# Optimization experiments

Measured on AMD Instinct MI355X. Metric: run time of the kernel, lower is better.

Reference implementation:

```python
import jax, jax.numpy as jnp
import numpy as np

N, E, T = 6144, 98304, 32
D_IN, D, D_FF, H, OUT = 128, 256, 256, 4, 2
DH = D // H
EPS = 1e-5


def setup_inputs() -> dict:
    key = jax.random.key(0)
    ks = jax.random.split(key, 24)
    s = 0.05
    inp = {
        "x": jax.random.normal(ks[0], (N, D_IN), jnp.float32),
        "edge_index": jax.random.randint(ks[1], (2, E), 0, N, jnp.int64 if jax.config.jax_enable_x64 else jnp.int32),
        "timesteps": jnp.sort(jax.random.randint(ks[2], (N,), 0, T)),
        "lin_l_w": jax.random.normal(ks[3], (D, D_IN), jnp.float32) * s,
        "lin_l_b": jnp.zeros((D,), jnp.float32),
        "lin_r_w": jax.random.normal(ks[4], (D, D_IN), jnp.float32) * s,
        "bn_gamma": jnp.ones((D,), jnp.float32),
        "bn_beta": jnp.zeros((D,), jnp.float32),
        "in_proj_w": jax.random.normal(ks[5], (2, 3 * D, D), jnp.float32) * s,
        "in_proj_b": jnp.zeros((2, 3 * D), jnp.float32),
        "out_w": jax.random.normal(ks[6], (2, D, D), jnp.float32) * s,
        "out_b": jnp.zeros((2, D), jnp.float32),
        "ff1_w": jax.random.normal(ks[7], (2, D_FF, D), jnp.float32) * s,
        "ff1_b": jnp.zeros((2, D_FF), jnp.float32),
        "ff2_w": jax.random.normal(ks[8], (2, D, D_FF), jnp.float32) * s,
        "ff2_b": jnp.zeros((2, D), jnp.float32),
        "ln1_g": jnp.ones((2, D), jnp.float32),
        "ln1_b": jnp.zeros((2, D), jnp.float32),
        "ln2_g": jnp.ones((2, D), jnp.float32),
        "ln2_b": jnp.zeros((2, D), jnp.float32),
        "cls_w": jax.random.normal(ks[9], (OUT, D), jnp.float32) * s,
        "cls_b": jnp.zeros((OUT,), jnp.float32),
    }
    return inp


def _layernorm(h, g, b):
    mu = jnp.mean(h, -1, keepdims=True)
    v = jnp.var(h, -1, keepdims=True)
    return (h - mu) * jax.lax.rsqrt(v + EPS) * g + b


def _forward(x, edge_index, timesteps, lin_l_w, lin_l_b, lin_r_w, bn_gamma, bn_beta,
             in_proj_w, in_proj_b, out_w, out_b, ff1_w, ff1_b, ff2_w, ff2_b,
             ln1_g, ln1_b, ln2_g, ln2_b, cls_w, cls_b):
    # SAGEConv (mean aggregation): out = lin_l(mean_{j->i} x_j) + lin_r(x_i)
    src, dst = edge_index[0], edge_index[1]
    agg = jax.ops.segment_sum(x[src], dst, num_segments=N)
    cnt = jax.ops.segment_sum(jnp.ones((E,), x.dtype), dst, num_segments=N)
    agg = agg / jnp.maximum(cnt, 1.0)[:, None]
    h = agg @ lin_l_w.T + lin_l_b + x @ lin_r_w.T

    # BatchNorm1d (training batch stats) + ReLU
    mu = jnp.mean(h, 0)
    var = jnp.var(h, 0)
    h = (h - mu) * jax.lax.rsqrt(var + EPS) * bn_gamma + bn_beta
    h = jax.nn.relu(h)

    # Per-timestep transformer == full attention with block-diagonal mask
    mask = timesteps[:, None] == timesteps[None, :]  # [N, N]
    neg = jnp.finfo(h.dtype).min

    for l in range(2):
        # self-attention (post-norm TransformerEncoderLayer)
        qkv = h @ in_proj_w[l].T + in_proj_b[l]             # [N, 3D]
        q, k, v = jnp.split(qkv, 3, axis=-1)
        q = q.reshape(N, H, DH).transpose(1, 0, 2)          # [H, N, DH]
        k = k.reshape(N, H, DH).transpose(1, 0, 2)
        v = v.reshape(N, H, DH).transpose(1, 0, 2)
        scores = jnp.einsum('hnd,hmd->hnm', q, k) / jnp.sqrt(jnp.asarray(DH, h.dtype))
        scores = jnp.where(mask[None], scores, neg)
        attn = jax.nn.softmax(scores, axis=-1)
        o = jnp.einsum('hnm,hmd->hnd', attn, v).transpose(1, 0, 2).reshape(N, D)
        o = o @ out_w[l].T + out_b[l]
        h = _layernorm(h + o, ln1_g[l], ln1_b[l])
        # FFN
        f = jax.nn.relu(h @ ff1_w[l].T + ff1_b[l]) @ ff2_w[l].T + ff2_b[l]
        h = _layernorm(h + f, ln2_g[l], ln2_b[l])

    return h @ cls_w.T + cls_b  # [N, OUT]


def reference(x, edge_index, timesteps, lin_l_w, lin_l_b, lin_r_w, bn_gamma, bn_beta,
              in_proj_w, in_proj_b, out_w, out_b, ff1_w, ff1_b, ff2_w, ff2_b,
              ln1_g, ln1_b, ln2_g, ln2_b, cls_w, cls_b):
    return _forward(x, edge_index, timesteps, lin_l_w, lin_l_b, lin_r_w, bn_gamma, bn_beta,
                    in_proj_w, in_proj_b, out_w, out_b, ff1_w, ff1_b, ff2_w, ff2_b,
                    ln1_g, ln1_b, ln2_g, ln2_b, cls_w, cls_b)
```

## Files before the change

kernel.cpp:

```cpp
#include <hip/hip_runtime.h>

#define NN   6144
#define EE   98304
#define DIN  128
#define DD   256
#define TT   32
#define NH   4
#define ATTN_Z 6
#define WROWS 3328

typedef __attribute__((ext_vector_type(8))) short short8;
typedef __attribute__((ext_vector_type(4))) float f32x4;
typedef unsigned short u16;

__device__ __forceinline__ float bf2f(u16 u) {
    return __uint_as_float(((unsigned)u) << 16);
}
__device__ __forceinline__ u16 f2bf(float f) {
    unsigned u = __float_as_uint(f);
    return (u16)((u + 0x7fffu + ((u >> 16) & 1u)) >> 16);
}
__device__ __forceinline__ unsigned pk2(float a, float b) {
    return (unsigned)f2bf(a) | ((unsigned)f2bf(b) << 16);
}
__device__ __forceinline__ float bnrelu(float v, float s, float q, float g, float b) {
    float mu = s * (1.0f / NN);
    float var = q * (1.0f / NN) - mu * mu;
    return fmaxf((v - mu) * rsqrtf(var + 1e-5f) * g + b, 0.0f);
}

__global__ void aml_zero_k(float* __restrict__ p) {
    p[blockIdx.x * 256 + threadIdx.x] = 0.0f;
}

__global__ void aml_hist_k(const int* __restrict__ ei, int* __restrict__ deg) {
    int e = blockIdx.x * 256 + threadIdx.x;
    if (e < EE) atomicAdd(&deg[ei[EE + e]], 1);
}

__global__ void aml_scan_k(const int* __restrict__ deg, int* __restrict__ rowptr,
                           int* __restrict__ cursor) {
    int t = threadIdx.x;
    int base = t * 24;
    int loc[24];
    int s = 0;
    #pragma unroll
    for (int j = 0; j < 24; ++j) { loc[j] = s; s += deg[base + j]; }
    __shared__ int part[256];
    part[t] = s;
    __syncthreads();
    for (int o = 1; o < 256; o <<= 1) {
        int v = (t >= o) ? part[t - o] : 0;
        __syncthreads();
        part[t] += v;
        __syncthreads();
    }
    int off = (t > 0) ? part[t - 1] : 0;
    #pragma unroll
    for (int j = 0; j < 24; ++j) {
        rowptr[base + j] = off + loc[j];
        cursor[base + j] = off + loc[j];
    }
    if (t == 255) rowptr[NN] = part[255];
}

__global__ void aml_scatter2_k(const int* __restrict__ ei, int* __restrict__ cursor,
                               int* __restrict__ eid) {
    int e = blockIdx.x * 256 + threadIdx.x;
    if (e >= EE) return;
    int slot = atomicAdd(&cursor[ei[EE + e]], 1);
    eid[slot] = ei[e];
}

__global__ void aml_gather_k(const float* __restrict__ x, const int* __restrict__ rowptr,
                             const int* __restrict__ eid, u16* __restrict__ ac) {
    int node = blockIdx.x * 4 + (threadIdx.x >> 6);
    int lane = threadIdx.x & 63;
    int p0 = rowptr[node], p1 = rowptr[node + 1];
    float ax = 0.f, ay = 0.f;
    int j = p0;
    for (; j + 1 < p1; j += 2) {
        int s0 = eid[j], s1 = eid[j + 1];
        float2 v0 = *(const float2*)(x + (size_t)s0 * DIN + lane * 2);
        float2 v1 = *(const float2*)(x + (size_t)s1 * DIN + lane * 2);
        ax += v0.x + v1.x; ay += v0.y + v1.y;
    }
    if (j < p1) {
        float2 v = *(const float2*)(x + (size_t)eid[j] * DIN + lane * 2);
        ax += v.x; ay += v.y;
    }
    float inv = 1.0f / fmaxf((float)(p1 - p0), 1.0f);
    float2 xr = *(const float2*)(x + (size_t)node * DIN + lane * 2);
    *(unsigned*)(ac + (size_t)node * DD + lane * 2) = pk2(ax * inv, ay * inv);
    *(unsigned*)(ac + (size_t)node * DD + DIN + lane * 2) = pk2(xr.x, xr.y);
}

__global__ void aml_prep_k(const float* __restrict__ lin_l_w, const float* __restrict__ lin_r_w,
                           const float* __restrict__ inp_w, const float* __restrict__ out_w,
                           const float* __restrict__ ff1_w, const float* __restrict__ ff2_w,
                           const int* __restrict__ ts, u16* __restrict__ wb,
                           int* __restrict__ offs) {
    int r = blockIdx.x;
    if (r == WROWS) {
        int t = threadIdx.x;
        if (t <= TT) {
            int lo = 0, hi = NN;
            while (lo < hi) { int mid = (lo + hi) >> 1; if (ts[mid] < t) lo = mid + 1; else hi = mid; }
            offs[t] = lo;
        }
        return;
    }
    int k = threadIdx.x;
    float v;
    if (r < 256) {
        v = (k < DIN) ? lin_l_w[r * DIN + k] : lin_r_w[r * DIN + (k - DIN)];
    } else {
        int r2 = r - 256;
        int l = r2 / 1536, r3 = r2 % 1536;
        const float* src; int rr;
        if (r3 < 768)       { src = inp_w + (size_t)l * 768 * DD; rr = r3; }
        else if (r3 < 1024) { src = out_w + (size_t)l * DD * DD;  rr = r3 - 768; }
        else if (r3 < 1280) { src = ff1_w + (size_t)l * DD * DD;  rr = r3 - 1024; }
        else                { src = ff2_w + (size_t)l * DD * DD;  rr = r3 - 1280; }
        v = src[(size_t)rr * DD + k];
    }
    wb[(size_t)r * DD + k] = f2bf(v);
}

template <int RELU, int AMODE, int CF32, int BNSTAT, int CT2>
__global__ __launch_bounds__(256)
void aml_gemm_k(const void* __restrict__ A, const u16* __restrict__ Wb,
                const float* __restrict__ bias, void* __restrict__ C, int M,
                float* __restrict__ stats, const float* __restrict__ bng,
                const float* __restrict__ bnb, float* __restrict__ h2) {
    __shared__ __align__(16) unsigned char lds[65536];
    const int t = threadIdx.x;
    const int brow = blockIdx.x * 64;
    const int bcol = blockIdx.y * (64 * CT2);

    #pragma unroll
    for (int p = 0; p < 8; ++p) {
        int c = t + p * 256;
        int row = c >> 5;
        int colb = (c & 31) * 16;
        int dst = row * 512 + (colb ^ ((row & 7) << 4));
        if (AMODE == 1) {
            const float* sA = (const float*)A + (size_t)(brow + row) * 256 + (c & 31) * 8;
            float4 a0 = *(const float4*)sA;
            float4 a1 = *(const float4*)(sA + 4);
            uint4 pa = { pk2(a0.x, a0.y), pk2(a0.z, a0.w), pk2(a1.x, a1.y), pk2(a1.z, a1.w) };
            *(uint4*)(lds + dst) = pa;
        } else if (AMODE == 2) {
            int d0 = (c & 31) * 8;
            const u16* sA = (const u16*)A + (size_t)(brow + row) * 256 + d0;
            uint4 raw = *(const uint4*)sA;
            const u16* rp = (const u16*)&raw;
            float av[8];
            #pragma unroll
            for (int i = 0; i < 8; ++i) {
                int d = d0 + i;
                av[i] = bnrelu(bf2f(rp[i]), stats[d], stats[DD + d], bng[d], bnb[d]);
            }
            if (blockIdx.y == 0) {
                float* hp = h2 + (size_t)(brow + row) * 256 + d0;
                *(float4*)hp = make_float4(av[0], av[1], av[2], av[3]);
                *(float4*)(hp + 4) = make_float4(av[4], av[5], av[6], av[7]);
            }
            uint4 pa = { pk2(av[0], av[1]), pk2(av[2], av[3]), pk2(av[4], av[5]), pk2(av[6], av[7]) };
            *(uint4*)(lds + dst) = pa;
        } else {
            const u16* sA = (const u16*)A + (size_t)(brow + row) * 256 + (c & 31) * 8;
            *(uint4*)(lds + dst) = *(const uint4*)sA;
        }
        *(uint4*)(lds + 32768 + dst) =
            *(const uint4*)(Wb + (size_t)(bcol + row) * 256 + (c & 31) * 8);
    }
    __syncthreads();

    const int wave = t >> 6, lane = t & 63;
    const int lrow = lane & 15, lk = lane >> 4;
    const int arow = wave * 16 + lrow;

    short8 af[8];
    #pragma unroll
    for (int ks = 0; ks < 8; ++ks) {
        int kbyte = ks * 64 + lk * 16;
        af[ks] = *(const short8*)(lds + arow * 512 + (kbyte ^ ((arow & 7) << 4)));
    }

    f32x4 acc[CT2][4] = {};
    #pragma unroll
    for (int c2 = 0; c2 < CT2; ++c2) {
        if (c2) {
            __syncthreads();
            #pragma unroll
            for (int p = 0; p < 8; ++p) {
                int c = t + p * 256;
                int row = c >> 5;
                int colb = (c & 31) * 16;
                int dst = 32768 + row * 512 + (colb ^ ((row & 7) << 4));
                *(uint4*)(lds + dst) =
                    *(const uint4*)(Wb + (size_t)(bcol + c2 * 64 + row) * 256 + (c & 31) * 8);
            }
            __syncthreads();
        }
        #pragma unroll
        for (int ks = 0; ks < 8; ++ks) {
            int kbyte = ks * 64 + lk * 16;
            #pragma unroll
            for (int ct = 0; ct < 4; ++ct) {
                int wrow = ct * 16 + lrow;
                short8 bf = *(const short8*)(lds + 32768 + wrow * 512 + (kbyte ^ ((wrow & 7) << 4)));
                acc[c2][ct] = __builtin_amdgcn_mfma_f32_16x16x32_bf16(af[ks], bf, acc[c2][ct], 0, 0, 0);
            }
        }
    }

    #pragma unroll
    for (int c2 = 0; c2 < CT2; ++c2) {
        #pragma unroll
        for (int ct = 0; ct < 4; ++ct) {
            int col = bcol + c2 * 64 + ct * 16 + lrow;
            float bv = bias[col];
            float s = 0.f, q = 0.f;
            #pragma unroll
            for (int r = 0; r < 4; ++r) {
                int grow = brow + wave * 16 + lk * 4 + r;
                float v = acc[c2][ct][r] + bv;
                if (RELU) v = fmaxf(v, 0.0f);
                if (CF32) ((float*)C)[(size_t)grow * M + col] = v;
                else      ((u16*)C)[(size_t)grow * M + col] = f2bf(v);
                if (BNSTAT) { s += v; q += v * v; }
            }
            if (BNSTAT) {
                s += __shfl_xor(s, 16); s += __shfl_xor(s, 32);
                q += __shfl_xor(q, 16); q += __shfl_xor(q, 32);
                if (lk == 0) {
                    atomicAdd(&stats[col], s);
                    atomicAdd(&stats[DD + col], q);
                }
            }
        }
    }
}

template <int CLS>
__global__ __launch_bounds__(256)
void aml_mega_k(const u16* __restrict__ A, const u16* __restrict__ Wb,
                const float* __restrict__ bias, float* __restrict__ h,
                u16* __restrict__ h2b,
                const float* __restrict__ g, const float* __restrict__ bv,
                const float* __restrict__ cls_w, const float* __restrict__ cls_b,
                float* __restrict__ out) {
    __shared__ __align__(16) unsigned char Al[8192];
    __shared__ __align__(16) unsigned char Wl[32768];
    __shared__ float reds[4][16], redq[4][16];
    __shared__ float redc[2][4][16];
    const int t = threadIdx.x;
    const int brow = blockIdx.x * 16;
    const int wave = t >> 6, lane = t & 63;
    const int lrow = lane & 15, lk = lane >> 4;
    const int wcol = wave * 64;

    #pragma unroll
    for (int p = 0; p < 2; ++p) {
        int c = t + p * 256;
        int row = c >> 5;
        int c8 = c & 31;
        const u16* sA = A + (size_t)(brow + row) * 256 + c8 * 8;
        *(uint4*)(Al + row * 512 + ((c8 * 16) ^ ((row & 7) << 4))) = *(const uint4*)sA;
    }

    short8 af[8];
    f32x4 acc[4] = {};
    for (int kc = 0; kc < 4; ++kc) {
        if (kc) __syncthreads();
        #pragma unroll
        for (int p = 0; p < 8; ++p) {
            int c = t + p * 256;
            int row = c >> 3, sub = c & 7;
            *(uint4*)(Wl + row * 128 + ((sub * 16) ^ ((row & 7) << 4))) =
                *(const uint4*)(Wb + (size_t)row * 256 + kc * 64 + sub * 8);
        }
        __syncthreads();
        if (kc == 0) {
            #pragma unroll
            for (int ks = 0; ks < 8; ++ks) {
                int kbyte = ks * 64 + lk * 16;
                af[ks] = *(const short8*)(Al + lrow * 512 + (kbyte ^ ((lrow & 7) << 4)));
            }
        }
        #pragma unroll
        for (int s = 0; s < 2; ++s) {
            int kb = s * 64 + lk * 16;
            #pragma unroll
            for (int ct = 0; ct < 4; ++ct) {
                int wrow = wcol + ct * 16 + lrow;
                short8 bf = *(const short8*)(Wl + wrow * 128 + (kb ^ ((wrow & 7) << 4)));
                acc[ct] = __builtin_amdgcn_mfma_f32_16x16x32_bf16(af[kc * 2 + s], bf, acc[ct], 0, 0, 0);
            }
        }
    }

    float s4[4] = {}, q4[4] = {};
    #pragma unroll
    for (int ct = 0; ct < 4; ++ct) {
        int col = wcol + ct * 16 + lrow;
        float bvv = bias[col];
        #pragma unroll
        for (int r = 0; r < 4; ++r) {
            int grow = brow + lk * 4 + r;
            float v = acc[ct][r] + bvv + h[(size_t)grow * DD + col];
            acc[ct][r] = v;
            s4[r] += v; q4[r] += v * v;
        }
    }
    #pragma unroll
    for (int off = 1; off < 16; off <<= 1) {
        #pragma unroll
        for (int r = 0; r < 4; ++r) {
            s4[r] += __shfl_xor(s4[r], off);
            q4[r] += __shfl_xor(q4[r], off);
        }
    }
    if (lrow == 0) {
        #pragma unroll
        for (int r = 0; r < 4; ++r) {
            reds[wave][lk * 4 + r] = s4[r];
            redq[wave][lk * 4 + r] = q4[r];
        }
    }
    __syncthreads();
    float mu[4], iv[4];
    #pragma unroll
    for (int r = 0; r < 4; ++r) {
        int rr = lk * 4 + r;
        float S = reds[0][rr] + reds[1][rr] + reds[2][rr] + reds[3][rr];
        float Q = redq[0][rr] + redq[1][rr] + redq[2][rr] + redq[3][rr];
        mu[r] = S * (1.0f / DD);
        iv[r] = rsqrtf(Q * (1.0f / DD) - mu[r] * mu[r] + 1e-5f);
    }
    float c0[4] = {}, c1[4] = {};
    #pragma unroll
    for (int ct = 0; ct < 4; ++ct) {
        int col = wcol + ct * 16 + lrow;
        float gv = g[col], bb = bv[col];
        float w0 = CLS ? cls_w[col] : 0.f;
        float w1 = CLS ? cls_w[DD + col] : 0.f;
        #pragma unroll
        for (int r = 0; r < 4; ++r) {
            int grow = brow + lk * 4 + r;
            float v = (acc[ct][r] - mu[r]) * iv[r] * gv + bb;
            h[(size_t)grow * DD + col] = v;
            h2b[(size_t)grow * DD + col] = f2bf(v);
            if (CLS) { c0[r] += v * w0; c1[r] += v * w1; }
        }
    }
    if (CLS) {
        #pragma unroll
        for (int off = 1; off < 16; off <<= 1) {
            #pragma unroll
            for (int r = 0; r < 4; ++r) {
                c0[r] += __shfl_xor(c0[r], off);
                c1[r] += __shfl_xor(c1[r], off);
            }
        }
        if (lrow == 0) {
            #pragma unroll
            for (int r = 0; r < 4; ++r) {
                redc[0][wave][lk * 4 + r] = c0[r];
                redc[1][wave][lk * 4 + r] = c1[r];
            }
        }
        __syncthreads();
        if (wave == 0 && lrow == 0) {
            float cb0 = cls_b[0], cb1 = cls_b[1];
            #pragma unroll
            for (int r = 0; r < 4; ++r) {
                int rr = lk * 4 + r;
                float o0 = redc[0][0][rr] + redc[0][1][rr] + redc[0][2][rr] + redc[0][3][rr];
                float o1 = redc[1][0][rr] + redc[1][1][rr] + redc[1][2][rr] + redc[1][3][rr];
                out[(brow + rr) * 2]     = o0 + cb0;
                out[(brow + rr) * 2 + 1] = o1 + cb1;
            }
        }
    }
}

__global__ __launch_bounds__(256)
void aml_attn_k(const u16* __restrict__ qkv, const int* __restrict__ offs,
                u16* __restrict__ o) {
    int tb = blockIdx.x, head = blockIdx.y, z = blockIdx.z;
    int start = offs[tb], end = offs[tb + 1];
    int S = end - start;
    if (S <= z * 64) return;
    int t = threadIdx.x, wave = t >> 6, lane = t & 63;
    int lq = lane & 15, lk = lane >> 4;
    int qoff = head * 64;

    __shared__ __align__(16) unsigned char Kl[8192];
    __shared__ __align__(16) unsigned char Vt[8192];
    __shared__ __align__(16) unsigned char Pl[4][2048];
    __shared__ float Ol[4][16][65];

    int qi = start + z * 64 + wave * 16 + lq;
    int qic = min(qi, end - 1);
    const u16* qp = qkv + (size_t)qic * 768 + qoff + lk * 8;
    short8 qf[2];
    qf[0] = *(const short8*)qp;
    qf[1] = *(const short8*)(qp + 32);

    float m = -1e30f, l = 0.f;
    f32x4 acc[4] = {};

    int ntile = (S + 63) >> 6;
    for (int tile = 0; tile < ntile; ++tile) {
        int jcnt = S - tile * 64; if (jcnt > 64) jcnt = 64;
        {
            int j = t >> 2, d0 = (t & 3) * 16;
            unsigned char* krow = Kl + j * 128;
            if (j < jcnt) {
                const u16* kp = qkv + (size_t)(start + tile * 64 + j) * 768 + 256 + qoff + d0;
                *(uint4*)(krow + ((d0 * 2) ^ ((j & 7) << 4))) = *(const uint4*)kp;
                *(uint4*)(krow + ((d0 * 2 + 16) ^ ((j & 7) << 4))) = *(const uint4*)(kp + 8);
                const u16* vp = kp + 256;
                #pragma unroll
                for (int i = 0; i < 16; ++i) {
                    int d = d0 + i;
                    *(u16*)(Vt + d * 128 + ((j * 2) ^ ((d & 7) << 4))) = vp[i];
                }
            } else {
                uint4 zz = { 0, 0, 0, 0 };
                *(uint4*)(krow + ((d0 * 2) ^ ((j & 7) << 4))) = zz;
                *(uint4*)(krow + ((d0 * 2 + 16) ^ ((j & 7) << 4))) = zz;
                #pragma unroll
                for (int i = 0; i < 16; ++i) {
                    int d = d0 + i;
                    *(u16*)(Vt + d * 128 + ((j * 2) ^ ((d & 7) << 4))) = 0;
                }
            }
        }
        __syncthreads();

        f32x4 sv[4];
        #pragma unroll
        for (int kt = 0; kt < 4; ++kt) {
            int kr = kt * 16 + lq;
            f32x4 s = {};
            #pragma unroll
            for (int ks = 0; ks < 2; ++ks) {
                short8 kf = *(const short8*)(Kl + kr * 128 + ((ks * 64 + lk * 16) ^ ((kr & 7) << 4)));
                s = __builtin_amdgcn_mfma_f32_16x16x32_bf16(kf, qf[ks], s, 0, 0, 0);
            }
            sv[kt] = s;
        }
        float pm = -1e30f;
        #pragma unroll
        for (int kt = 0; kt < 4; ++kt) {
            #pragma unroll
            for (int r = 0; r < 4; ++r) {
                int kk = tile * 64 + kt * 16 + lk * 4 + r;
                float s = (kk < S) ? sv[kt][r] * 0.125f : -1e30f;
                sv[kt][r] = s;
                pm = fmaxf(pm, s);
            }
        }
        pm = fmaxf(pm, __shfl_xor(pm, 16));
        pm = fmaxf(pm, __shfl_xor(pm, 32));
        float mn = fmaxf(m, pm);
        float corr = __expf(m - mn);
        m = mn;
        float ps = 0.f;
        #pragma unroll
        for (int kt = 0; kt < 4; ++kt) {
            #pragma unroll
            for (int r = 0; r < 4; ++r) {
                float p = __expf(sv[kt][r] - mn);
                sv[kt][r] = p;
                ps += p;
            }
            uint2 w = { pk2(sv[kt][0], sv[kt][1]), pk2(sv[kt][2], sv[kt][3]) };
            *(uint2*)(Pl[wave] + lq * 128 + ((kt * 32 + lk * 8) ^ ((lq & 7) << 4))) = w;
        }
        ps += __shfl_xor(ps, 16);
        ps += __shfl_xor(ps, 32);
        l = l * corr + ps;
        #pragma unroll
        for (int dt = 0; dt < 4; ++dt) {
            #pragma unroll
            for (int r = 0; r < 4; ++r) acc[dt][r] *= corr;
        }
        #pragma unroll
        for (int ks = 0; ks < 2; ++ks) {
            short8 pf = *(const short8*)(Pl[wave] + lq * 128 + ((ks * 64 + lk * 16) ^ ((lq & 7) << 4)));
            #pragma unroll
            for (int dt = 0; dt < 4; ++dt) {
                int dr = dt * 16 + lq;
                short8 vf = *(const short8*)(Vt + dr * 128 + ((ks * 64 + lk * 16) ^ ((dr & 7) << 4)));
                acc[dt] = __builtin_amdgcn_mfma_f32_16x16x32_bf16(vf, pf, acc[dt], 0, 0, 0);
            }
        }
        __syncthreads();
    }

    float linv = 1.0f / l;
    #pragma unroll
    for (int dt = 0; dt < 4; ++dt) {
        #pragma unroll
        for (int r = 0; r < 4; ++r)
            Ol[wave][lq][dt * 16 + lk * 4 + r] = acc[dt][r] * linv;
    }
    int q2 = lane >> 2, c2 = lane & 3;
    int qg = start + z * 64 + wave * 16 + q2;
    if (qg < end) {
        u16* op = o + (size_t)qg * DD + qoff + c2 * 16;
        const float* sp = &Ol[wave][q2][c2 * 16];
        #pragma unroll
        for (int i = 0; i < 8; ++i)
            ((unsigned*)op)[i] = pk2(sp[2 * i], sp[2 * i + 1]);
    }
}

extern "C" void kernel_launch(void* const* d_in, const int* in_sizes, int n_in,
                              void* d_out, int out_size, void* d_ws, size_t ws_size,
                              hipStream_t stream) {
    const float* x       = (const float*)d_in[0];
    const int*   ei      = (const int*)d_in[1];
    const int*   ts      = (const int*)d_in[2];
    const float* lin_l_w = (const float*)d_in[3];
    const float* lin_l_b = (const float*)d_in[4];
    const float* lin_r_w = (const float*)d_in[5];
    const float* bn_g    = (const float*)d_in[6];
    const float* bn_b    = (const float*)d_in[7];
    const float* inp_w   = (const float*)d_in[8];
    const float* inp_b   = (const float*)d_in[9];
    const float* out_w   = (const float*)d_in[10];
    const float* out_b   = (const float*)d_in[11];
    const float* ff1_w   = (const float*)d_in[12];
    const float* ff1_b   = (const float*)d_in[13];
    const float* ff2_w   = (const float*)d_in[14];
    const float* ff2_b   = (const float*)d_in[15];
    const float* ln1_g   = (const float*)d_in[16];
    const float* ln1_b   = (const float*)d_in[17];
    const float* ln2_g   = (const float*)d_in[18];
    const float* ln2_b   = (const float*)d_in[19];
    const float* cls_w   = (const float*)d_in[20];
    const float* cls_b   = (const float*)d_in[21];

    float* ws     = (float*)d_ws;
    float* stats  = ws;
    int*   deg    = (int*)(stats + 512);
    int*   rowptr = deg + NN;
    int*   cursor = rowptr + NN + 4;
    int*   eid    = cursor + NN;
    int*   offs   = eid + EE;
    u16*   wb     = (u16*)(offs + 64);
    u16*   hb     = wb + (size_t)WROWS * 256;
    float* h2     = (float*)(hb + (size_t)NN * DD);
    u16*   h2b    = (u16*)(h2 + (size_t)NN * DD);
    u16*   qkv    = h2b + (size_t)NN * DD;
    u16*   t1     = qkv + (size_t)NN * 768;
    u16*   ac     = qkv;

    const u16* wb_cat = wb;
    const u16* wb_inp[2] = { wb + (size_t)(256) * 256,        wb + (size_t)(256 + 1536) * 256 };
    const u16* wb_out[2] = { wb + (size_t)(256 + 768) * 256,  wb + (size_t)(256 + 1536 + 768) * 256 };
    const u16* wb_ff1[2] = { wb + (size_t)(256 + 1024) * 256, wb + (size_t)(256 + 1536 + 1024) * 256 };
    const u16* wb_ff2[2] = { wb + (size_t)(256 + 1280) * 256, wb + (size_t)(256 + 1536 + 1280) * 256 };

    aml_zero_k<<<26, 256, 0, stream>>>(stats);
    aml_hist_k<<<EE / 256, 256, 0, stream>>>(ei, deg);
    aml_scan_k<<<1, 256, 0, stream>>>(deg, rowptr, cursor);
    aml_scatter2_k<<<EE / 256, 256, 0, stream>>>(ei, cursor, eid);
    aml_gather_k<<<NN / 4, 256, 0, stream>>>(x, rowptr, eid, ac);
    aml_prep_k<<<WROWS + 1, 256, 0, stream>>>(lin_l_w, lin_r_w, inp_w, out_w, ff1_w, ff2_w,
                                              ts, wb, offs);
    aml_gemm_k<0, 0, 0, 1, 2><<<dim3(NN / 64, 2), 256, 0, stream>>>(
        ac, wb_cat, lin_l_b, hb, DD, stats, nullptr, nullptr, nullptr);

    for (int l = 0; l < 2; ++l) {
        if (l == 0)
            aml_gemm_k<0, 2, 0, 0, 2><<<dim3(NN / 64, 6), 256, 0, stream>>>(
                hb, wb_inp[0], inp_b, qkv, 768, stats, bn_g, bn_b, h2);
        else
            aml_gemm_k<0, 0, 0, 0, 2><<<dim3(NN / 64, 6), 256, 0, stream>>>(
                h2b, wb_inp[1], inp_b + 768, qkv, 768, nullptr, nullptr, nullptr, nullptr);
        aml_attn_k<<<dim3(TT, NH, ATTN_Z), 256, 0, stream>>>(qkv, offs, t1);
        aml_mega_k<0><<<NN / 16, 256, 0, stream>>>(t1, wb_out[l], out_b + (size_t)l * DD, h2, h2b,
                                                   ln1_g + (size_t)l * DD, ln1_b + (size_t)l * DD,
                                                   nullptr, nullptr, nullptr);
        aml_gemm_k<1, 0, 0, 0, 2><<<dim3(NN / 64, 2), 256, 0, stream>>>(
            h2b, wb_ff1[l], ff1_b + (size_t)l * DD, t1, DD, nullptr, nullptr, nullptr, nullptr);
        if (l == 0)
            aml_mega_k<0><<<NN / 16, 256, 0, stream>>>(t1, wb_ff2[0], ff2_b, h2, h2b,
                                                       ln2_g, ln2_b, nullptr, nullptr, nullptr);
        else
            aml_mega_k<1><<<NN / 16, 256, 0, stream>>>(t1, wb_ff2[1], ff2_b + DD, h2, h2b,
                                                       ln2_g + DD, ln2_b + DD,
                                                       cls_w, cls_b, (float*)d_out);
    }
}
```

Before: 166.6 us.

## Fuse out-proj, LN1, FFN, LN2 and next-layer QKV into one tail kernel

Replaces the per-layer sequence of out-projection+LN, FF1 GEMM, FF2+LN, and next-layer QKV GEMM with a single kernel per 16-row block that chains all GEMMs through LDS. This removes several launches and the global round trips of intermediate activations (h2b, t1 for FF1). The cost is that each 16-row block reloads all weight matrices from L2, including three 256x256 QKV chunks, and runs with low per-block arithmetic intensity, so it may lose the wider tiling of the old QKV GEMM.

```diff
diff --git a/kernel.cpp b/kernel.cpp
--- a/kernel.cpp
+++ b/kernel.cpp
@@ -144,13 +144,7 @@
         int row = c >> 5;
         int colb = (c & 31) * 16;
         int dst = row * 512 + (colb ^ ((row & 7) << 4));
-        if (AMODE == 1) {
-            const float* sA = (const float*)A + (size_t)(brow + row) * 256 + (c & 31) * 8;
-            float4 a0 = *(const float4*)sA;
-            float4 a1 = *(const float4*)(sA + 4);
-            uint4 pa = { pk2(a0.x, a0.y), pk2(a0.z, a0.w), pk2(a1.x, a1.y), pk2(a1.z, a1.w) };
-            *(uint4*)(lds + dst) = pa;
-        } else if (AMODE == 2) {
+        if (AMODE == 2) {
             int d0 = (c & 31) * 8;
             const u16* sA = (const u16*)A + (size_t)(brow + row) * 256 + d0;
             uint4 raw = *(const uint4*)sA;
@@ -244,12 +238,84 @@
     }
 }
 
-template <int CLS>
+#define TAIL_GEMM(WPTR, LOADA)                                                            \
+    _Pragma("unroll")                                                                     \
+    for (int kc = 0; kc < 4; ++kc) {                                                      \
+        __syncthreads();                                                                  \
+        _Pragma("unroll")                                                                 \
+        for (int p = 0; p < 8; ++p) {                                                     \
+            int c = t + p * 256;                                                          \
+            int row = c >> 3, sub = c & 7;                                                \
+            *(uint4*)(Wl + row * 128 + ((sub * 16) ^ ((row & 7) << 4))) =                 \
+                *(const uint4*)((WPTR) + (size_t)row * 256 + kc * 64 + sub * 8);          \
+        }                                                                                 \
+        __syncthreads();                                                                  \
+        if ((LOADA) && kc == 0) {                                                         \
+            _Pragma("unroll")                                                             \
+            for (int ks = 0; ks < 8; ++ks) {                                              \
+                int kbyte = ks * 64 + lk * 16;                                            \
+                af[ks] = *(const short8*)(Al + lrow * 512 + (kbyte ^ ((lrow & 7) << 4))); \
+            }                                                                             \
+        }                                                                                 \
+        _Pragma("unroll")                                                                 \
+        for (int s = 0; s < 2; ++s) {                                                     \
+            int kb = s * 64 + lk * 16;                                                    \
+            _Pragma("unroll")                                                             \
+            for (int ct = 0; ct < 4; ++ct) {                                              \
+                int wrow = wcol + ct * 16 + lrow;                                         \
+                short8 bf = *(const short8*)(Wl + wrow * 128 + (kb ^ ((wrow & 7) << 4))); \
+                acc[ct] = __builtin_amdgcn_mfma_f32_16x16x32_bf16(af[kc * 2 + s], bf,     \
+                                                                  acc[ct], 0, 0, 0);      \
+            }                                                                             \
+        }                                                                                 \
+    }
+
+#define WRITE_AL(VARR)                                                                    \
+    _Pragma("unroll")                                                                     \
+    for (int ct = 0; ct < 4; ++ct) {                                                      \
+        _Pragma("unroll")                                                                 \
+        for (int r = 0; r < 4; ++r) {                                                     \
+            int row = lk * 4 + r, col = wcol + ct * 16 + lrow;                            \
+            *(u16*)(Al + row * 512 + ((col * 2) ^ ((row & 7) << 4))) = f2bf(VARR[ct][r]); \
+        }                                                                                 \
+    }
+
+#define ROW_LN_STATS(S4, Q4, MU, IV)                                                      \
+    _Pragma("unroll")                                                                     \
+    for (int off = 1; off < 16; off <<= 1) {                                              \
+        _Pragma("unroll")                                                                 \
+        for (int r = 0; r < 4; ++r) {                                                     \
+            S4[r] += __shfl_xor(S4[r], off);                                              \
+            Q4[r] += __shfl_xor(Q4[r], off);                                              \
+        }                                                                                 \
+    }                                                                                     \
+    if (lrow == 0) {                                                                      \
+        _Pragma("unroll")                                                                 \
+        for (int r = 0; r < 4; ++r) {                                                     \
+            reds[wave][lk * 4 + r] = S4[r];                                               \
+            redq[wave][lk * 4 + r] = Q4[r];                                               \
+        }                                                                                 \
+    }                                                                                     \
+    __syncthreads();                                                                      \
+    _Pragma("unroll")                                                                     \
+    for (int r = 0; r < 4; ++r) {                                                         \
+        int rr = lk * 4 + r;                                                              \
+        float S = reds[0][rr] + reds[1][rr] + reds[2][rr] + reds[3][rr];                  \
+        float Q = redq[0][rr] + redq[1][rr] + redq[2][rr] + redq[3][rr];                  \
+        MU[r] = S * (1.0f / DD);                                                          \
+        IV[r] = rsqrtf(Q * (1.0f / DD) - MU[r] * MU[r] + 1e-5f);                          \
+    }
+
+template <int LAST>
 __global__ __launch_bounds__(256)
-void aml_mega_k(const u16* __restrict__ A, const u16* __restrict__ Wb,
-                const float* __restrict__ bias, float* __restrict__ h,
-                u16* __restrict__ h2b,
-                const float* __restrict__ g, const float* __restrict__ bv,
+void aml_tail_k(const u16* __restrict__ A, float* __restrict__ h2,
+                const u16* __restrict__ Wout, const float* __restrict__ bout,
+                const float* __restrict__ g1, const float* __restrict__ b1,
+                const u16* __restrict__ Wff1, const float* __restrict__ bff1,
+                const u16* __restrict__ Wff2, const float* __restrict__ bff2,
+                const float* __restrict__ g2, const float* __restrict__ b2,
+                const u16* __restrict__ Wq, const float* __restrict__ bq,
+                u16* __restrict__ qkv,
                 const float* __restrict__ cls_w, const float* __restrict__ cls_b,
                 float* __restrict__ out) {
     __shared__ __align__(16) unsigned char Al[8192];
@@ -265,98 +331,130 @@
     #pragma unroll
     for (int p = 0; p < 2; ++p) {
         int c = t + p * 256;
-        int row = c >> 5;
-        int c8 = c & 31;
-        const u16* sA = A + (size_t)(brow + row) * 256 + c8 * 8;
-        *(uint4*)(Al + row * 512 + ((c8 * 16) ^ ((row & 7) << 4))) = *(const uint4*)sA;
+        int row = c >> 5, c8 = c & 31;
+        *(uint4*)(Al + row * 512 + ((c8 * 16) ^ ((row & 7) << 4))) =
+            *(const uint4*)(A + (size_t)(brow + row) * 256 + c8 * 8);
     }
 
     short8 af[8];
-    f32x4 acc[4] = {};
-    for (int kc = 0; kc < 4; ++kc) {
-        if (kc) __syncthreads();
-        #pragma unroll
-        for (int p = 0; p < 8; ++p) {
-            int c = t + p * 256;
-            int row = c >> 3, sub = c & 7;
-            *(uint4*)(Wl + row * 128 + ((sub * 16) ^ ((row & 7) << 4))) =
-                *(const uint4*)(Wb + (size_t)row * 256 + kc * 64 + sub * 8);
+    f32x4 acc[4];
+
+    #pragma unroll
+    for (int ct = 0; ct < 4; ++ct) acc[ct] = (f32x4){0.f, 0.f, 0.f, 0.f};
+    TAIL_GEMM(Wout, true)
+
+    float ln1v[4][4];
+    {
+        float s4[4] = {}, q4[4] = {};
+        #pragma unroll
+        for (int ct = 0; ct < 4; ++ct) {
+            int col = wcol + ct * 16 + lrow;
+            float bvv = bout[col];
+            #pragma unroll
+            for (int r = 0; r < 4; ++r) {
+                int grow = brow + lk * 4 + r;
+                float v = acc[ct][r] + bvv + h2[(size_t)grow * DD + col];
+                acc[ct][r] = v;
+                s4[r] += v; q4[r] += v * v;
+            }
+        }
+        float mu[4], iv[4];
+        ROW_LN_STATS(s4, q4, mu, iv)
+        #pragma unroll
+        for (int ct = 0; ct < 4; ++ct) {
+            int col = wcol + ct * 16 + lrow;
+            float gv = g1[col], bb = b1[col];
+            #pragma unroll
+            for (int r = 0; r < 4; ++r)
+                ln1v[ct][r] = (acc[ct][r] - mu[r]) * iv[r] * gv + bb;
+        }
+        WRITE_AL(ln1v)
+    }
+
+    #pragma unroll
+    for (int ct = 0; ct < 4; ++ct) acc[ct] = (f32x4){0.f, 0.f, 0.f, 0.f};
+    TAIL_GEMM(Wff1, true)
+    {
+        float fv[4][4];
+        #pragma unroll
+        for (int ct = 0; ct < 4; ++ct) {
+            int col = wcol + ct * 16 + lrow;
+            float bvv = bff1[col];
+            #pragma unroll
+            for (int r = 0; r < 4; ++r)
+                fv[ct][r] = fmaxf(acc[ct][r] + bvv, 0.0f);
         }
         __syncthreads();
-        if (kc == 0) {
-            #pragma unroll
-            for (int ks = 0; ks < 8; ++ks) {
-                int kbyte = ks * 64 + lk * 16;
-                af[ks] = *(const short8*)(Al + lrow * 512 + (kbyte ^ ((lrow & 7) << 4)));
-            }
-        }
-        #pragma unroll
-        for (int s = 0; s < 2; ++s) {
-            int kb = s * 64 + lk * 16;
+        WRITE_AL(fv)
+    }
+
+    #pragma unroll
+    for (int ct = 0; ct < 4; ++ct) acc[ct] = (f32x4){0.f, 0.f, 0.f, 0.f};
+    TAIL_GEMM(Wff2, true)
+    float ln2v[4][4];
+    {
+        float s4[4] = {}, q4[4] = {};
+        #pragma unroll
+        for (int ct = 0; ct < 4; ++ct) {
+            int col = wcol + ct * 16 + lrow;
+            float bvv = bff2[col];
+            #pragma unroll
+            for (int r = 0; r < 4; ++r) {
+                float v = acc[ct][r] + bvv + ln1v[ct][r];
+                acc[ct][r] = v;
+                s4[r] += v; q4[r] += v * v;
+            }
+        }
+        float mu[4], iv[4];
+        ROW_LN_STATS(s4, q4, mu, iv)
+        #pragma unroll
+        for (int ct = 0; ct < 4; ++ct) {
+            int col = wcol + ct * 16 + lrow;
+            float gv = g2[col], bb = b2[col];
+            #pragma unroll
+            for (int r = 0; r < 4; ++r) {
+                float v = (acc[ct][r] - mu[r]) * iv[r] * gv + bb;
+                ln2v[ct][r] = v;
+                if (!LAST) {
+                    int grow = brow + lk * 4 + r;
+                    h2[(size_t)grow * DD + col] = v;
+                }
+            }
+        }
+        if (!LAST) {
+            WRITE_AL(ln2v)
+        }
+    }
+
+    if (!LAST) {
+        #pragma unroll
+        for (int cg = 0; cg < 3; ++cg) {
+            #pragma unroll
+            for (int ct = 0; ct < 4; ++ct) acc[ct] = (f32x4){0.f, 0.f, 0.f, 0.f};
+            TAIL_GEMM(Wq + (size_t)cg * 256 * 256, cg == 0)
             #pragma unroll
             for (int ct = 0; ct < 4; ++ct) {
-                int wrow = wcol + ct * 16 + lrow;
-                short8 bf = *(const short8*)(Wl + wrow * 128 + (kb ^ ((wrow & 7) << 4)));
-                acc[ct] = __builtin_amdgcn_mfma_f32_16x16x32_bf16(af[kc * 2 + s], bf, acc[ct], 0, 0, 0);
-            }
-        }
-    }
-
-    float s4[4] = {}, q4[4] = {};
-    #pragma unroll
-    for (int ct = 0; ct < 4; ++ct) {
-        int col = wcol + ct * 16 + lrow;
-        float bvv = bias[col];
-        #pragma unroll
-        for (int r = 0; r < 4; ++r) {
-            int grow = brow + lk * 4 + r;
-            float v = acc[ct][r] + bvv + h[(size_t)grow * DD + col];
-            acc[ct][r] = v;
-            s4[r] += v; q4[r] += v * v;
-        }
-    }
-    #pragma unroll
-    for (int off = 1; off < 16; off <<= 1) {
-        #pragma unroll
-        for (int r = 0; r < 4; ++r) {
-            s4[r] += __shfl_xor(s4[r], off);
-            q4[r] += __shfl_xor(q4[r], off);
-        }
-    }
-    if (lrow == 0) {
-        #pragma unroll
-        for (int r = 0; r < 4; ++r) {
-            reds[wave][lk * 4 + r] = s4[r];
-            redq[wave][lk * 4 + r] = q4[r];
-        }
-    }
-    __syncthreads();
-    float mu[4], iv[4];
-    #pragma unroll
-    for (int r = 0; r < 4; ++r) {
-        int rr = lk * 4 + r;
-        float S = reds[0][rr] + reds[1][rr] + reds[2][rr] + reds[3][rr];
-        float Q = redq[0][rr] + redq[1][rr] + redq[2][rr] + redq[3][rr];
-        mu[r] = S * (1.0f / DD);
-        iv[r] = rsqrtf(Q * (1.0f / DD) - mu[r] * mu[r] + 1e-5f);
-    }
-    float c0[4] = {}, c1[4] = {};
-    #pragma unroll
-    for (int ct = 0; ct < 4; ++ct) {
-        int col = wcol + ct * 16 + lrow;
-        float gv = g[col], bb = bv[col];
-        float w0 = CLS ? cls_w[col] : 0.f;
-        float w1 = CLS ? cls_w[DD + col] : 0.f;
-        #pragma unroll
-        for (int r = 0; r < 4; ++r) {
-            int grow = brow + lk * 4 + r;
-            float v = (acc[ct][r] - mu[r]) * iv[r] * gv + bb;
-            h[(size_t)grow * DD + col] = v;
-            h2b[(size_t)grow * DD + col] = f2bf(v);
-            if (CLS) { c0[r] += v * w0; c1[r] += v * w1; }
-        }
-    }
-    if (CLS) {
+                int col = cg * 256 + wcol + ct * 16 + lrow;
+                float bvv = bq[col];
+                #pragma unroll
+                for (int r = 0; r < 4; ++r) {
+                    int grow = brow + lk * 4 + r;
+                    qkv[(size_t)grow * 768 + col] = f2bf(acc[ct][r] + bvv);
+                }
+            }
+        }
+    } else {
+        float c0[4] = {}, c1[4] = {};
+        #pragma unroll
+        for (int ct = 0; ct < 4; ++ct) {
+            int col = wcol + ct * 16 + lrow;
+            float w0 = cls_w[col], w1 = cls_w[DD + col];
+            #pragma unroll
+            for (int r = 0; r < 4; ++r) {
+                c0[r] += ln2v[ct][r] * w0;
+                c1[r] += ln2v[ct][r] * w1;
+            }
+        }
         #pragma unroll
         for (int off = 1; off < 16; off <<= 1) {
             #pragma unroll
@@ -557,8 +655,7 @@
     u16*   wb     = (u16*)(offs + 64);
     u16*   hb     = wb + (size_t)WROWS * 256;
     float* h2     = (float*)(hb + (size_t)NN * DD);
-    u16*   h2b    = (u16*)(h2 + (size_t)NN * DD);
-    u16*   qkv    = h2b + (size_t)NN * DD;
+    u16*   qkv    = (u16*)(h2 + (size_t)NN * DD);
     u16*   t1     = qkv + (size_t)NN * 768;
     u16*   ac     = qkv;
 
@@ -577,26 +674,18 @@
                                               ts, wb, offs);
     aml_gemm_k<0, 0, 0, 1, 2><<<dim3(NN / 64, 2), 256, 0, stream>>>(
         ac, wb_cat, lin_l_b, hb, DD, stats, nullptr, nullptr, nullptr);
-
-    for (int l = 0; l < 2; ++l) {
-        if (l == 0)
-            aml_gemm_k<0, 2, 0, 0, 2><<<dim3(NN / 64, 6), 256, 0, stream>>>(
-                hb, wb_inp[0], inp_b, qkv, 768, stats, bn_g, bn_b, h2);
-        else
-            aml_gemm_k<0, 0, 0, 0, 2><<<dim3(NN / 64, 6), 256, 0, stream>>>(
-                h2b, wb_inp[1], inp_b + 768, qkv, 768, nullptr, nullptr, nullptr, nullptr);
-        aml_attn_k<<<dim3(TT, NH, ATTN_Z), 256, 0, stream>>>(qkv, offs, t1);
-        aml_mega_k<0><<<NN / 16, 256, 0, stream>>>(t1, wb_out[l], out_b + (size_t)l * DD, h2, h2b,
-                                                   ln1_g + (size_t)l * DD, ln1_b + (size_t)l * DD,
-                                                   nullptr, nullptr, nullptr);
-        aml_gemm_k<1, 0, 0, 0, 2><<<dim3(NN / 64, 2), 256, 0, stream>>>(
-            h2b, wb_ff1[l], ff1_b + (size_t)l * DD, t1, DD, nullptr, nullptr, nullptr, nullptr);
-        if (l == 0)
-            aml_mega_k<0><<<NN / 16, 256, 0, stream>>>(t1, wb_ff2[0], ff2_b, h2, h2b,
-                                                       ln2_g, ln2_b, nullptr, nullptr, nullptr);
-        else
-            aml_mega_k<1><<<NN / 16, 256, 0, stream>>>(t1, wb_ff2[1], ff2_b + DD, h2, h2b,
-                                                       ln2_g + DD, ln2_b + DD,
-                                                       cls_w, cls_b, (float*)d_out);
-    }
-}
+    aml_gemm_k<0, 2, 0, 0, 2><<<dim3(NN / 64, 6), 256, 0, stream>>>(
+        hb, wb_inp[0], inp_b, qkv, 768, stats, bn_g, bn_b, h2);
+
+    aml_attn_k<<<dim3(TT, NH, ATTN_Z), 256, 0, stream>>>(qkv, offs, t1);
+    aml_tail_k<0><<<NN / 16, 256, 0, stream>>>(
+        t1, h2, wb_out[0], out_b, ln1_g, ln1_b,
+        wb_ff1[0], ff1_b, wb_ff2[0], ff2_b, ln2_g, ln2_b,
+        wb_inp[1], inp_b + 768, qkv, nullptr, nullptr, nullptr);
+
+    aml_attn_k<<<dim3(TT, NH, ATTN_Z), 256, 0, stream>>>(qkv, offs, t1);
+    aml_tail_k<1><<<NN / 16, 256, 0, stream>>>(
+        t1, h2, wb_out[1], out_b + DD, ln1_g + DD, ln1_b + DD,
+        wb_ff1[1], ff1_b + DD, wb_ff2[1], ff2_b + DD, ln2_g + DD, ln2_b + DD,
+        nullptr, nullptr, nullptr, cls_w, cls_b, (float*)d_out);
+}
```

Measured after the change: 154.9 us. 7.0% less time.
